# Kernel optimization log

Hardware: AMD Instinct MI355X
Metric: run time of the kernel (lower is better)

The kernel has to match this reference:

```python
import jax, jax.numpy as jnp
import numpy as np
import math

# ---------- real Clebsch-Gordan coupling tables (computed once, tiny) ----------
def _cg(j1, m1, j2, m2, j3, m3):
    if m1 + m2 != m3 or j3 < abs(j1 - j2) or j3 > j1 + j2:
        return 0.0
    f = math.factorial
    pre = ((2 * j3 + 1) * f(j3 + j1 - j2) * f(j3 - j1 + j2) * f(j1 + j2 - j3) / f(j1 + j2 + j3 + 1)) ** 0.5
    pre *= (f(j3 + m3) * f(j3 - m3) * f(j1 - m1) * f(j1 + m1) * f(j2 - m2) * f(j2 + m2)) ** 0.5
    s = 0.0
    for k in range(0, j1 + j2 - j3 + 1):
        d = (k, j1 + j2 - j3 - k, j1 - m1 - k, j2 + m2 - k, j3 - j2 + m1 + k, j3 - j1 - m2 + k)
        if min(d) < 0:
            continue
        den = 1
        for t in d:
            den *= f(t)
        s += (-1) ** k / den
    return pre * s

def _Q(l):  # complex->real spherical-harmonic change of basis
    Q = np.zeros((2 * l + 1, 2 * l + 1), dtype=complex)
    Q[l, l] = 1.0
    s = 2 ** -0.5
    for m in range(1, l + 1):
        Q[l + m, l + m] = (-1) ** m * s
        Q[l + m, l - m] = s
        Q[l - m, l + m] = -1j * (-1) ** m * s
        Q[l - m, l - m] = 1j * s
    return Q

def _K(l1, l2, l3):  # real coupling tensor [2l3+1, 2l1+1, 2l2+1]
    C = np.zeros((2 * l3 + 1, 2 * l1 + 1, 2 * l2 + 1), dtype=complex)
    for M3 in range(-l3, l3 + 1):
        for M1 in range(-l1, l1 + 1):
            for M2 in range(-l2, l2 + 1):
                C[M3 + l3, M1 + l1, M2 + l2] = _cg(l1, M1, l2, M2, l3, M3)
    K = np.einsum('cC,aA,bB,CAB->cab', _Q(l3).conj(), _Q(l1), _Q(l2), C)
    K = K.imag if np.abs(K.imag).max() > np.abs(K.real).max() else K.real
    return np.asarray(K, dtype=np.float32)

# the 9 'uvu' instructions (in_l, edge_l, out_l) with multiplicities (weight_numel=144)
_PATHS = [(0, 0, 0), (0, 2, 2), (1, 0, 1), (1, 2, 1), (1, 2, 2), (2, 0, 2), (2, 2, 0), (2, 2, 1), (2, 2, 2)]
_KT = [jnp.asarray(_K(*p)) for p in _PATHS]
_MULS = [32, 32, 16, 16, 16, 8, 8, 8, 8]
_SPLITS = np.cumsum(_MULS)[:-1].tolist()
NEI = 8
EPS = 1e-5

def _sh(u):  # component-normalized real SH of unit vectors, l=0..2 (m order -l..l, l=1 -> y,z,x)
    x, y, z = u[:, 0], u[:, 1], u[:, 2]
    sh0 = jnp.ones_like(x)[:, None]
    sh1 = np.float32(3 ** 0.5) * jnp.stack([y, z, x], -1)
    s15 = np.float32(15 ** 0.5)
    s5 = np.float32(5 ** 0.5)
    sh2 = jnp.stack([s15 * x * y, s15 * y * z, 0.5 * s5 * (3 * z * z - 1.0), s15 * x * z, 0.5 * s15 * (x * x - y * y)], -1)
    return sh0, sh1, sh2

def _path(xs, sh, wp, Kt):  # xs [E,u,2l1+1], sh [E,2l2+1], Kt [2l3+1,2l1+1,2l2+1] -> [E,u,2l3+1]
    return jnp.einsum('eui,ej,oij->euo', xs, sh, Kt) * wp[None, :, None]

def _layer(x0, x1, x2, pos, src, dst, w, W0, W1, W2, bw0, bb0, bw1, bw2, N):
    ev = pos[dst] - pos[src]
    u = ev / (jnp.linalg.norm(ev, axis=1, keepdims=True) + 1e-12)
    sh0, sh1, sh2 = _sh(u)
    s0 = x0[src][:, :, None]  # [E,32,1]
    s1 = x1[src]              # [E,16,3]
    s2 = x2[src]              # [E,8,5]
    ws = jnp.split(w, _SPLITS)
    p1 = _path(s0, sh0, ws[0], _KT[0])
    p2 = _path(s0, sh2, ws[1], _KT[1])
    p3 = _path(s1, sh0, ws[2], _KT[2])
    p4 = _path(s1, sh2, ws[3], _KT[3])
    p5 = _path(s1, sh2, ws[4], _KT[4])
    p6 = _path(s2, sh0, ws[5], _KT[5])
    p7 = _path(s2, sh2, ws[6], _KT[6])
    p8 = _path(s2, sh2, ws[7], _KT[7])
    p9 = _path(s2, sh2, ws[8], _KT[8])
    m0 = jnp.concatenate([p1, p7], 1)          # [E,40,1]
    m1 = jnp.concatenate([p3, p4, p8], 1)      # [E,40,3]
    m2 = jnp.concatenate([p2, p5, p6, p9], 1)  # [E,64,5]
    a0 = jax.ops.segment_sum(m0, dst, num_segments=N)
    a1 = jax.ops.segment_sum(m1, dst, num_segments=N)
    a2 = jax.ops.segment_sum(m2, dst, num_segments=N)
    y0 = (a0[:, :, 0] @ W0) * np.float32(1.0 / 40 ** 0.5)
    y1 = jnp.einsum('num,uv->nvm', a1, W1) * np.float32(1.0 / 40 ** 0.5)
    y2 = jnp.einsum('num,uv->nvm', a2, W2) * np.float32(1.0 / 64 ** 0.5)
    # equivariant batchnorm (training stats): scalars -> standard BN, l>0 -> norm BN
    f = y0 - y0.mean(0)
    y0 = f / jnp.sqrt((f * f).mean(0) + EPS) * bw0 + bb0
    y1 = y1 / jnp.sqrt((y1 * y1).mean(axis=(0, 2)) + EPS)[None, :, None] * bw1[None, :, None]
    y2 = y2 / jnp.sqrt((y2 * y2).mean(axis=(0, 2)) + EPS)[None, :, None] * bw2[None, :, None]
    return y0, y1, y2

def _forward(positions, W_emb, tp_w, lin_W0, lin_W1, lin_W2, bn_w0, bn_b0, bn_w1, bn_w2, Wf1, Wf2, bf2, Wf3, bf3):
    B, P, _ = positions.shape
    N = B * P
    pos = positions.reshape(N, 3)
    # kNN graph from dense cdist + topk (indices are not differentiated)
    pg = jax.lax.stop_gradient(pos)
    sq = jnp.sum(pg * pg, 1)
    d2 = sq[:, None] + sq[None, :] - 2.0 * (pg @ pg.T)
    _, idx = jax.lax.top_k(-d2, NEI + 1)  # smallest distances; col 0 is self
    src = jnp.repeat(jnp.arange(N), NEI)
    dst = idx[:, 1:].reshape(-1)
    x0 = jnp.ones((N, 1), jnp.float32) @ W_emb  # embedding: only 0e->0e path exists
    x1 = jnp.zeros((N, 16, 3), jnp.float32)
    x2 = jnp.zeros((N, 8, 5), jnp.float32)
    for l in range(3):
        y0, y1, y2 = _layer(x0, x1, x2, pos, src, dst, tp_w[l], lin_W0[l], lin_W1[l], lin_W2[l],
                            bn_w0[l], bn_b0[l], bn_w1[l], bn_w2[l], N)
        x0 = jax.nn.relu(y0) + x0
        x1 = jax.nn.relu(y1) + x1
        x2 = jax.nn.relu(y2) + x2
    h = jax.nn.relu((x0 @ Wf1) * np.float32(1.0 / 32 ** 0.5))  # scalar part -> 32x0e
    h = jax.nn.relu(h @ Wf2 + bf2)
    out = (h @ Wf3 + bf3).reshape(B, P, 2)
    return out

def setup_inputs() -> dict:
    key = jax.random.key(0)
    ks = jax.random.split(key, 16)
    B, P = 4, 2048
    return {
        'positions': jax.random.normal(ks[0], (B, P, 3), jnp.float32) * 3.0,
        'W_emb': jax.random.normal(ks[1], (1, 32), jnp.float32),
        'tp_w': jax.random.normal(ks[2], (3, 144), jnp.float32),
        'lin_W0': jax.random.normal(ks[3], (3, 40, 32), jnp.float32),
        'lin_W1': jax.random.normal(ks[4], (3, 40, 16), jnp.float32),
        'lin_W2': jax.random.normal(ks[5], (3, 64, 8), jnp.float32),
        'bn_w0': 1.0 + 0.05 * jax.random.normal(ks[6], (3, 32), jnp.float32),
        'bn_b0': jnp.zeros((3, 32), jnp.float32),
        'bn_w1': 1.0 + 0.05 * jax.random.normal(ks[7], (3, 16), jnp.float32),
        'bn_w2': 1.0 + 0.05 * jax.random.normal(ks[8], (3, 8), jnp.float32),
        'Wf1': jax.random.normal(ks[9], (32, 32), jnp.float32),
        'Wf2': jax.random.normal(ks[10], (32, 16), jnp.float32) * 0.2,
        'bf2': jax.random.normal(ks[11], (16,), jnp.float32) * 0.1,
        'Wf3': jax.random.normal(ks[12], (16, 2), jnp.float32) * 0.2,
        'bf3': jax.random.normal(ks[13], (2,), jnp.float32) * 0.1,
    }

def reference(positions, W_emb, tp_w, lin_W0, lin_W1, lin_W2, bn_w0, bn_b0, bn_w1, bn_w2, Wf1, Wf2, bf2, Wf3, bf3):
    return _forward(positions, W_emb, tp_w, lin_W0, lin_W1, lin_W2, bn_w0, bn_b0, bn_w1, bn_w2, Wf1, Wf2, bf2, Wf3, bf3)
```

## Files before the change

### kernel.cpp

```cpp
#include <hip/hip_runtime.h>
#include <math.h>

#define NN 8192
#define REV_CAP 48
#define KNN_CAP 384
#define PF 12

static const size_t OFF_K     = 0;
static const size_t OFF_CNT   = 512;
static const size_t OFF_REV   = 8704;
static const size_t OFF_STATS = 401920;
static const size_t OFF_XF    = 406528;
static const size_t OFF_YF    = 1389568;
static const size_t WS_FLOATS = 2372608;

__device__ double dfact(int n){ double r=1.0; for(int i=2;i<=n;++i) r*=(double)i; return r; }

__device__ double dcg(int j1,int m1,int j2,int m2,int j3,int m3){
  if (m1+m2!=m3) return 0.0;
  if (j3 < abs(j1-j2) || j3 > j1+j2) return 0.0;
  double pre = sqrt((double)(2*j3+1)*dfact(j3+j1-j2)*dfact(j3-j1+j2)*dfact(j1+j2-j3)/dfact(j1+j2+j3+1));
  pre *= sqrt(dfact(j3+m3)*dfact(j3-m3)*dfact(j1-m1)*dfact(j1+m1)*dfact(j2-m2)*dfact(j2+m2));
  double s=0.0;
  for(int k=0;k<=j1+j2-j3;++k){
    int d1=j1+j2-j3-k, d2=j1-m1-k, d3=j2+m2-k, d4=j3-j2+m1+k, d5=j3-j1-m2+k;
    if(d1<0||d2<0||d3<0||d4<0||d5<0) continue;
    double den = dfact(k)*dfact(d1)*dfact(d2)*dfact(d3)*dfact(d4)*dfact(d5);
    s += ((k&1)? -1.0: 1.0)/den;
  }
  return pre*s;
}

__device__ int qrow(int l,int r,int* col,double* re,double* im){
  const double s = 0.70710678118654752440;
  if (r==l){ col[0]=l; re[0]=1.0; im[0]=0.0; return 1; }
  if (r>l){ int m=r-l;
    col[0]=l+m; re[0]=((m&1)?-s:s); im[0]=0.0;
    col[1]=l-m; re[1]=s;            im[1]=0.0;
  } else { int m=l-r;
    col[0]=l+m; re[0]=0.0; im[0]=((m&1)? s : -s);
    col[1]=l-m; re[1]=0.0; im[1]=s;
  }
  return 2;
}

__global__ __launch_bounds__(256) void k_setup(const float* __restrict__ pos,
        const float* __restrict__ W_emb, float* __restrict__ Kbuf,
        float* __restrict__ xf,
        float* __restrict__ xs, float* __restrict__ ys, float* __restrict__ zs,
        float* __restrict__ qs,
        int* __restrict__ cnt, float* __restrict__ stats){
  int idx = blockIdx.x*256 + threadIdx.x;
  if (idx < 983040) { const int c = idx%120; xf[idx] = (c<32)? W_emb[c] : 0.f; return; }
  idx -= 983040;
  if (idx < 8192) {
    const float x=pos[3*idx], y=pos[3*idx+1], z=pos[3*idx+2];
    xs[idx]=x; ys[idx]=y; zs[idx]=z; qs[idx]=0.5f*(x*x+y*y+z*z);
    return;
  }
  idx -= 8192;
  if (idx < 8192) { cnt[idx]=0; return; }
  idx -= 8192;
  if (idx < 3072) { stats[idx]=0.f; return; }
  idx -= 3072;
  if (idx >= 405) return;

  const int tid = idx;
  const int sizes[9]={1,25,9,45,75,25,25,75,125};
  const int l1s[9]={0,0,1,1,1,2,2,2,2};
  const int l2s[9]={0,2,0,2,2,0,2,2,2};
  const int l3s[9]={0,2,1,1,2,2,0,1,2};
  int p=0, rem=tid;
  for(p=0;p<9;++p){ if(rem < sizes[p]) break; rem -= sizes[p]; }
  const int l1=l1s[p], l2=l2s[p], l3=l3s[p];
  const int n1=2*l1+1, n2=2*l2+1;
  const int c = rem/(n1*n2); const int r2 = rem%(n1*n2); const int a=r2/n2; const int b=r2%n2;

  int c3[2],c1[2],c2[2]; double re3[2],im3[2],re1[2],im1[2],re2[2],im2[2];
  const int nc3 = qrow(l3,c,c3,re3,im3);
  const int nc1 = qrow(l1,a,c1,re1,im1);
  const int nc2 = qrow(l2,b,c2,re2,im2);

  double accRe=0, accIm=0;
  for(int i3=0;i3<nc3;++i3){
    const double q3re=re3[i3], q3im=-im3[i3];
    for(int i1=0;i1<nc1;++i1){
      const double pre_re = q3re*re1[i1] - q3im*im1[i1];
      const double pre_im = q3re*im1[i1] + q3im*re1[i1];
      for(int i2=0;i2<nc2;++i2){
        const double cgv = dcg(l1, c1[i1]-l1, l2, c2[i2]-l2, l3, c3[i3]-l3);
        if (cgv==0.0) continue;
        accRe += (pre_re*re2[i2] - pre_im*im2[i2])*cgv;
        accIm += (pre_re*im2[i2] + pre_im*re2[i2])*cgv;
      }
    }
  }
  const bool useImag = ((l1+l2+l3)&1)!=0;
  Kbuf[tid] = (float)(useImag? accIm : accRe);
}

__device__ __forceinline__ unsigned fkey(float f){
  const unsigned b = __float_as_uint(f);
  return (b & 0x80000000u) ? ~b : (b | 0x80000000u);
}

#define RSELECT_PUSH(KMAX) do{ \
  unsigned P = 0u; int need = 9; \
  _Pragma("unroll 1") \
  for(int bit=31; bit>=0; --bit){ \
    const unsigned pref = P >> bit; \
    int c0 = 0; \
    _Pragma("unroll") \
    for(int k=0;k<KMAX;++k) c0 += __popcll(__ballot((ku[k]>>bit)==pref)); \
    if (need > c0){ need -= c0; P |= (1u<<bit); } \
  } \
  int c_eq = 0; \
  _Pragma("unroll") \
  for(int k=0;k<KMAX;++k) c_eq += __popcll(__ballot(ku[k]==P)); \
  bool tsel[KMAX]; \
  _Pragma("unroll") \
  for(int k=0;k<KMAX;++k) tsel[k] = (ku[k]==P); \
  if (c_eq > need){ \
    _Pragma("unroll") \
    for(int k=0;k<KMAX;++k) tsel[k]=false; \
    for(int r=0;r<need;++r){ \
      int mid = 0x7fffffff; \
      _Pragma("unroll") \
      for(int k=0;k<KMAX;++k) if (ku[k]==P && !tsel[k] && il[k]<mid) mid = il[k]; \
      _Pragma("unroll") \
      for(int s=32;s>0;s>>=1){ const int om = __shfl_xor(mid,s,64); mid = (om<mid)? om : mid; } \
      _Pragma("unroll") \
      for(int k=0;k<KMAX;++k) if (ku[k]==P && il[k]==mid) tsel[k]=true; \
    } \
  } \
  _Pragma("unroll") \
  for(int k=0;k<KMAX;++k){ \
    const bool take = (ku[k] < P) || tsel[k]; \
    const int ix = il[k]; \
    if (take && ix != node){ \
      int cpos = atomicAdd(&cnt[ix],1); \
      if (cpos < REV_CAP) rev[ix*REV_CAP + cpos] = node; \
    } \
  } \
}while(0)

__global__ __launch_bounds__(256, 8) void k_knn8(const float* __restrict__ xs,
                                              const float* __restrict__ ys,
                                              const float* __restrict__ zs,
                                              const float* __restrict__ qs,
                                              int* __restrict__ cnt, int* __restrict__ rev){
  const int lane = threadIdx.x & 63;
  const int w    = threadIdx.x >> 6;
  const int node = blockIdx.x*4 + w;
  __shared__ float sdist[4][KNN_CAP];
  __shared__ int   sidx[4][KNN_CAP];
  __shared__ int   scount[4];
  if (threadIdx.x < 4) scount[threadIdx.x]=0;
  __syncthreads();

  const float px = xs[node], py = ys[node], pz = zs[node];

  float m1 = INFINITY, m2 = INFINITY;
  for(int c=0;c<4;++c){
    const int base = (c*64 + lane)*4;
    const float4 fx = *(const float4*)(xs + base);
    const float4 fy = *(const float4*)(ys + base);
    const float4 fz = *(const float4*)(zs + base);
    const float4 fq = *(const float4*)(qs + base);
    float ss[4];
    ss[0] = fmaf(-px,fx.x, fmaf(-py,fy.x, fmaf(-pz,fz.x, fq.x)));
    ss[1] = fmaf(-px,fx.y, fmaf(-py,fy.y, fmaf(-pz,fz.y, fq.y)));
    ss[2] = fmaf(-px,fx.z, fmaf(-py,fy.z, fmaf(-pz,fz.z, fq.z)));
    ss[3] = fmaf(-px,fx.w, fmaf(-py,fy.w, fmaf(-pz,fz.w, fq.w)));
    #pragma unroll
    for(int q=0;q<4;++q){
      const float hi = fmaxf(m1, ss[q]);
      m1 = fminf(m1, ss[q]);
      m2 = fminf(m2, hi);
    }
  }
  {
    const unsigned kk1 = fkey(m1), kk2 = fkey(m2);
    unsigned P = 0u; int need = 9;
    #pragma unroll 1
    for(int bit=31; bit>=0; --bit){
      const unsigned pref = P >> bit;
      const int c0 = __popcll(__ballot((kk1>>bit)==pref)) + __popcll(__ballot((kk2>>bit)==pref));
      if (need > c0){ need -= c0; P |= (1u<<bit); }
    }
    m1 = __uint_as_float((P & 0x80000000u) ? (P & 0x7fffffffu) : ~P);
  }
  const float T = m1;

  {
    const int b0 = lane*4;
    float4 nfx = *(const float4*)(xs + b0);
    float4 nfy = *(const float4*)(ys + b0);
    float4 nfz = *(const float4*)(zs + b0);
    float4 nfq = *(const float4*)(qs + b0);
    for(int c=0;c<32;++c){
      const float4 fx=nfx, fy=nfy, fz=nfz, fq=nfq;
      const int cbase = (c*64 + lane)*4;
      if (c<31){
        const int nb2 = ((c+1)*64 + lane)*4;
        nfx = *(const float4*)(xs + nb2);
        nfy = *(const float4*)(ys + nb2);
        nfz = *(const float4*)(zs + nb2);
        nfq = *(const float4*)(qs + nb2);
      }
      float ss[4];
      ss[0] = fmaf(-px,fx.x, fmaf(-py,fy.x, fmaf(-pz,fz.x, fq.x)));
      ss[1] = fmaf(-px,fx.y, fmaf(-py,fy.y, fmaf(-pz,fz.y, fq.y)));
      ss[2] = fmaf(-px,fx.z, fmaf(-py,fy.z, fmaf(-pz,fz.z, fq.z)));
      ss[3] = fmaf(-px,fx.w, fmaf(-py,fy.w, fmaf(-pz,fz.w, fq.w)));
      #pragma unroll
      for(int q=0;q<4;++q){
        if (ss[q] <= T){
          int pos = atomicAdd(&scount[w],1);
          if (pos < KNN_CAP){ sdist[w][pos]=ss[q]; sidx[w][pos]=cbase+q; }
        }
      }
    }
  }
  __syncthreads();

  int m = scount[w]; if (m > KNN_CAP) m = KNN_CAP;
  unsigned ku[KNN_CAP/64]; int il[KNN_CAP/64];
  #pragma unroll
  for(int k=0;k<KNN_CAP/64;++k){
    const int j = lane + 64*k;
    if (j < m){ ku[k]=fkey(sdist[w][j]); il[k]=sidx[w][j]; }
    else      { ku[k]=0xffffffffu;       il[k]=0x7fffffff; }
  }
  if (m <= 128) RSELECT_PUSH(2);
  else          RSELECT_PUSH(6);
}

__global__ __launch_bounds__(256) void k_msg(
  const float* __restrict__ pos,
  const int* __restrict__ cnt, const int* __restrict__ rev,
  const float* __restrict__ Kbuf,
  const float* __restrict__ xf,
  const float* __restrict__ tpw,
  const float* __restrict__ W0, const float* __restrict__ W1, const float* __restrict__ W2,
  float* __restrict__ pA, float* __restrict__ pB,
  float* __restrict__ yf)
{
  const int t = threadIdx.x;
  const int w = t >> 6;
  const int lane = t & 63;
  const int n = blockIdx.x*4 + w;

  __shared__ float KL[405];
  __shared__ float TW[144];
  __shared__ float momP[4][120];
  __shared__ float momS[4][600];
  __shared__ float aS[4][480];
  __shared__ int   eIdx[4][REV_CAP];
  __shared__ float eSh[4][5][REV_CAP];
  __shared__ float bA[32], bB[96];
  for(int q=t;q<405;q+=256) KL[q]=Kbuf[q];
  for(int q=t;q<144;q+=256) TW[q]=tpw[q];
  if (t<96){ bB[t]=0.f; if(t<32) bA[t]=0.f; }

  const int deg0 = cnt[n];
  const int deg = (deg0<REV_CAP)? deg0 : REV_CAP;
  const float pnx=pos[3*n], pny=pos[3*n+1], pnz=pos[3*n+2];
  const float s15 = 3.8729833462f, s5c = 2.2360679775f;
  if (lane < deg){
    const int i = rev[n*REV_CAP+lane];
    eIdx[w][lane] = i;
    const float ex = pnx - pos[3*i], ey = pny - pos[3*i+1], ez = pnz - pos[3*i+2];
    const float rn = sqrtf(ex*ex+ey*ey+ez*ez) + 1e-12f;
    const float ux=ex/rn, uy=ey/rn, uz=ez/rn;
    eSh[w][0][lane]=s15*ux*uy;
    eSh[w][1][lane]=s15*uy*uz;
    eSh[w][2][lane]=0.5f*s5c*(3.f*uz*uz-1.f);
    eSh[w][3][lane]=s15*ux*uz;
    eSh[w][4][lane]=0.5f*s15*(ux*ux-uy*uy);
  }
  __syncthreads();

  const int c0 = lane*2;
  float mp0=0.f, mp1=0.f;
  float ms0[5], ms1[5];
  #pragma unroll
  for(int j=0;j<5;++j){ ms0[j]=0.f; ms1[j]=0.f; }

  int idxr[PF];
  #pragma unroll
  for(int k=0;k<PF;++k) idxr[k] = (k<deg)? eIdx[w][k] : 0;
  float2 fr[PF];
  if (lane<60){
    #pragma unroll
    for(int k=0;k<PF;++k) fr[k] = *(const float2*)(xf + (size_t)idxr[k]*120 + c0);
  }
  #pragma unroll
  for(int k=0;k<PF;++k){
    if (k<deg){
      const float sh0=eSh[w][0][k], sh1=eSh[w][1][k], sh2=eSh[w][2][k];
      const float sh3=eSh[w][3][k], sh4=eSh[w][4][k];
      if (lane<60){
        const float2 f = fr[k];
        mp0 += f.x; mp1 += f.y;
        ms0[0]+=f.x*sh0; ms0[1]+=f.x*sh1; ms0[2]+=f.x*sh2; ms0[3]+=f.x*sh3; ms0[4]+=f.x*sh4;
        ms1[0]+=f.y*sh0; ms1[1]+=f.y*sh1; ms1[2]+=f.y*sh2; ms1[3]+=f.y*sh3; ms1[4]+=f.y*sh4;
      }
    }
  }
  for(int e=PF;e<deg;++e){
    const int i = eIdx[w][e];
    const float sh0=eSh[w][0][e], sh1=eSh[w][1][e], sh2=eSh[w][2][e];
    const float sh3=eSh[w][3][e], sh4=eSh[w][4][e];
    if (lane<60){
      const float2 f = *(const float2*)(xf + (size_t)i*120 + c0);
      mp0 += f.x; mp1 += f.y;
      ms0[0]+=f.x*sh0; ms0[1]+=f.x*sh1; ms0[2]+=f.x*sh2; ms0[3]+=f.x*sh3; ms0[4]+=f.x*sh4;
      ms1[0]+=f.y*sh0; ms1[1]+=f.y*sh1; ms1[2]+=f.y*sh2; ms1[3]+=f.y*sh3; ms1[4]+=f.y*sh4;
    }
  }
  if (lane<60){
    momP[w][c0]=mp0; momP[w][c0+1]=mp1;
    #pragma unroll
    for(int j=0;j<5;++j){ momS[w][c0*5+j]=ms0[j]; momS[w][(c0+1)*5+j]=ms1[j]; }
  }
  __syncthreads();

  float acc[14];
  #pragma unroll
  for(int k=0;k<14;++k) acc[k]=0.f;

  if (lane<32){
    const int u=lane;
    const float rw0=TW[u], rw1=TW[32+u];
    acc[0] = rw0 * KL[0] * momP[w][u];
    float m0s[5];
    #pragma unroll
    for(int j=0;j<5;++j) m0s[j]=momS[w][u*5+j];
    #pragma unroll
    for(int o=0;o<5;++o){ float g=0.f;
      #pragma unroll
      for(int j=0;j<5;++j) g += KL[1+o*5+j]*m0s[j];
      acc[1+o] = rw1*g; }
  } else if (lane<48){
    const int u=lane-32;
    const float rw0=TW[64+u], rw1=TW[80+u], rw2=TW[96+u];
    float m1p[3], m1s[3][5];
    #pragma unroll
    for(int i=0;i<3;++i){
      m1p[i]=momP[w][32+u*3+i];
      #pragma unroll
      for(int j=0;j<5;++j) m1s[i][j]=momS[w][(32+u*3+i)*5+j];
    }
    #pragma unroll
    for(int o=0;o<3;++o){ float g=0.f;
      #pragma unroll
      for(int i=0;i<3;++i) g += KL[26+o*3+i]*m1p[i];
      acc[o]=rw0*g; }
    #pragma unroll
    for(int o=0;o<3;++o){ float g=0.f;
      #pragma unroll
      for(int i=0;i<3;++i)
        #pragma unroll
        for(int j=0;j<5;++j) g += KL[35+(o*3+i)*5+j]*m1s[i][j];
      acc[3+o]=rw1*g; }
    #pragma unroll
    for(int o=0;o<5;++o){ float g=0.f;
      #pragma unroll
      for(int i=0;i<3;++i)
        #pragma unroll
        for(int j=0;j<5;++j) g += KL[80+(o*3+i)*5+j]*m1s[i][j];
      acc[6+o]=rw2*g; }
  } else if (lane<56){
    const int u=lane-48;
    const float rw0=TW[112+u], rw1=TW[120+u], rw2=TW[128+u], rw3=TW[136+u];
    float m2p[5], m2s[5][5];
    #pragma unroll
    for(int i=0;i<5;++i){
      m2p[i]=momP[w][80+u*5+i];
      #pragma unroll
      for(int j=0;j<5;++j) m2s[i][j]=momS[w][(80+u*5+i)*5+j];
    }
    #pragma unroll
    for(int o=0;o<5;++o){ float g=0.f;
      #pragma unroll
      for(int i=0;i<5;++i) g += KL[155+o*5+i]*m2p[i];
      acc[o]=rw0*g; }
    { float g=0.f;
      #pragma unroll
      for(int i=0;i<5;++i)
        #pragma unroll
        for(int j=0;j<5;++j) g += KL[180+i*5+j]*m2s[i][j];
      acc[5]=rw1*g; }
    #pragma unroll
    for(int o=0;o<3;++o){ float g=0.f;
      #pragma unroll
      for(int i=0;i<5;++i)
        #pragma unroll
        for(int j=0;j<5;++j) g += KL[205+(o*5+i)*5+j]*m2s[i][j];
      acc[6+o]=rw2*g; }
    #pragma unroll
    for(int o=0;o<5;++o){ float g=0.f;
      #pragma unroll
      for(int i=0;i<5;++i)
        #pragma unroll
        for(int j=0;j<5;++j) g += KL[280+(o*5+i)*5+j]*m2s[i][j];
      acc[9+o]=rw3*g; }
  }

  if (lane<32){
    aS[w][lane] = acc[0];
    #pragma unroll
    for(int o=0;o<5;++o) aS[w][160 + lane*5+o] = acc[1+o];
  } else if (lane<48){
    const int uu=lane-32;
    #pragma unroll
    for(int m=0;m<3;++m){ aS[w][40 + uu*3+m] = acc[m]; aS[w][40 + (16+uu)*3+m] = acc[3+m]; }
    #pragma unroll
    for(int o=0;o<5;++o) aS[w][160 + (32+uu)*5+o] = acc[6+o];
  } else if (lane<56){
    const int uu=lane-48;
    aS[w][32+uu] = acc[5];
    #pragma unroll
    for(int m=0;m<3;++m) aS[w][40 + (32+uu)*3+m] = acc[6+m];
    #pragma unroll
    for(int o=0;o<5;++o){ aS[w][160 + (48+uu)*5+o] = acc[o]; aS[w][160 + (56+uu)*5+o] = acc[9+o]; }
  }
  __syncthreads();

  const float inv40 = 0.15811388300841896660f;
  for(int q=lane;q<120;q+=64){
    float out; int chan;
    if (q<32){
      float g=0.f;
      for(int uu=0;uu<40;++uu) g += aS[w][uu]*W0[uu*32+q];
      out = g*inv40; chan = q;
    } else if (q<80){
      const int e=q-32, v=e/3, m=e%3;
      float g=0.f;
      for(int uu=0;uu<40;++uu) g += aS[w][40+uu*3+m]*W1[uu*16+v];
      out = g*inv40; chan = 32+v;
    } else {
      const int e=q-80, tt=e/5, m=e%5;
      float g=0.f;
      for(int uu=0;uu<64;++uu) g += aS[w][160+uu*5+m]*W2[uu*8+tt];
      out = g*0.125f; chan = 48+tt;
    }
    yf[(size_t)n*120+q] = out;
    atomicAdd(&bB[chan], out*out);
    if (q<32) atomicAdd(&bA[q], out);
  }
  __syncthreads();
  if (t<96){
    const int slot = blockIdx.x & 7;
    atomicAdd(&pB[slot*96 + t], bB[t]);
    if (t<32) atomicAdd(&pA[slot*32 + t], bA[t]);
  }
}

__global__ __launch_bounds__(256) void k_norm(const float* __restrict__ yf,
                       const float* __restrict__ pA, const float* __restrict__ pB,
                       const float* __restrict__ bw0,const float* __restrict__ bb0,
                       const float* __restrict__ bw1,const float* __restrict__ bw2,
                       float* __restrict__ xf){
  __shared__ float sc[96], sf[32];
  const int t = threadIdx.x;
  if (t<96){
    float sB=0.f;
    #pragma unroll
    for(int k=0;k<8;++k) sB += pB[k*96+t];
    float scale;
    if (t<32){
      float sA=0.f;
      #pragma unroll
      for(int k=0;k<8;++k) sA += pA[k*32+t];
      const float mean = sA*(1.f/8192.f);
      const float var  = sB*(1.f/8192.f) - mean*mean;
      const float inv  = 1.f/sqrtf(var+1e-5f);
      scale = bw0[t]*inv;
      sf[t] = bb0[t] - mean*scale;
    } else if (t<48){
      scale = bw1[t-32]/sqrtf(sB*(1.f/(8192.f*3.f))+1e-5f);
    } else {
      scale = bw2[t-48]/sqrtf(sB*(1.f/(8192.f*5.f))+1e-5f);
    }
    sc[t]=scale;
  }
  __syncthreads();
  const int idx = blockIdx.x*256 + t;
  if (idx >= NN*120) return;
  const int c = idx%120;
  const int chan = (c<32)? c : ((c<80)? 32+(c-32)/3 : 48+(c-80)/5);
  const float v = yf[idx]*sc[chan] + ((c<32)? sf[c] : 0.f);
  xf[idx] += fmaxf(v,0.f);
}

__global__ __launch_bounds__(256) void k_normmlp(const float* __restrict__ yf,
                                             const float* __restrict__ xf,
                                             const float* __restrict__ pA, const float* __restrict__ pB,
                                             const float* __restrict__ bw0,const float* __restrict__ bb0,
                                             const float* __restrict__ Wf1,const float* __restrict__ Wf2,
                                             const float* __restrict__ bf2,const float* __restrict__ Wf3,
                                             const float* __restrict__ bf3, float* __restrict__ out){
  __shared__ float w1[1024], w2[512], w3[32], b2[16], b3[2], sc0[32], sf0[32];
  const int t=threadIdx.x;
  for(int q=t;q<1024;q+=256) w1[q]=Wf1[q];
  for(int q=t;q<512;q+=256)  w2[q]=Wf2[q];
  if(t<32) w3[t]=Wf3[t];
  if(t<16) b2[t]=bf2[t];
  if(t<2)  b3[t]=bf3[t];
  if(t<32){
    float sA=0.f, sB=0.f;
    #pragma unroll
    for(int k=0;k<8;++k){ sA += pA[k*32+t]; sB += pB[k*96+t]; }
    const float mean = sA*(1.f/8192.f);
    const float var  = sB*(1.f/8192.f) - mean*mean;
    const float inv  = 1.f/sqrtf(var+1e-5f);
    sc0[t] = bw0[t]*inv;
    sf0[t] = bb0[t] - mean*sc0[t];
  }
  __syncthreads();
  const int n = blockIdx.x*256+t;
  if(n>=NN) return;
  float xv[32];
  #pragma unroll
  for(int k=0;k<32;++k){
    const float v = yf[(size_t)n*120+k]*sc0[k] + sf0[k];
    xv[k] = xf[(size_t)n*120+k] + fmaxf(v,0.f);
  }
  const float inv32 = 0.17677669529663688110f;
  float h1[32];
  #pragma unroll 4
  for(int c=0;c<32;++c){ float g=0.f;
    #pragma unroll
    for(int k=0;k<32;++k) g+=xv[k]*w1[k*32+c];
    h1[c]=fmaxf(g*inv32,0.f); }
  float h2[16];
  #pragma unroll 4
  for(int c=0;c<16;++c){ float g=b2[c];
    #pragma unroll
    for(int k=0;k<32;++k) g+=h1[k]*w2[k*16+c];
    h2[c]=fmaxf(g,0.f); }
  #pragma unroll
  for(int m=0;m<2;++m){ float g=b3[m];
    #pragma unroll
    for(int k=0;k<16;++k) g+=h2[k]*w3[k*2+m];
    out[n*2+m]=g; }
}

extern "C" void kernel_launch(void* const* d_in, const int* in_sizes, int n_in,
                              void* d_out, int out_size, void* d_ws, size_t ws_size,
                              hipStream_t stream) {
  const float* positions = (const float*)d_in[0];
  const float* W_emb  = (const float*)d_in[1];
  const float* tp_w   = (const float*)d_in[2];
  const float* lin_W0 = (const float*)d_in[3];
  const float* lin_W1 = (const float*)d_in[4];
  const float* lin_W2 = (const float*)d_in[5];
  const float* bn_w0  = (const float*)d_in[6];
  const float* bn_b0  = (const float*)d_in[7];
  const float* bn_w1  = (const float*)d_in[8];
  const float* bn_w2  = (const float*)d_in[9];
  const float* Wf1 = (const float*)d_in[10];
  const float* Wf2 = (const float*)d_in[11];
  const float* bf2 = (const float*)d_in[12];
  const float* Wf3 = (const float*)d_in[13];
  const float* bf3 = (const float*)d_in[14];

  if (ws_size < WS_FLOATS*sizeof(float)) return;

  float* ws    = (float*)d_ws;
  float* Kbuf  = ws + OFF_K;
  int*   cnt   = (int*)(ws + OFF_CNT);
  int*   rev   = (int*)(ws + OFF_REV);
  float* stats = ws + OFF_STATS;
  float* xf = ws + OFF_XF;
  float* yf = ws + OFF_YF;

  float* xs = yf;
  float* ysA = yf + NN;
  float* zs = yf + 2*NN;
  float* qs = yf + 3*NN;

  k_setup<<<3918,256,0,stream>>>(positions, W_emb, Kbuf, xf, xs, ysA, zs, qs, cnt, stats);
  k_knn8<<<NN/4,256,0,stream>>>(xs, ysA, zs, qs, cnt, rev);

  for(int l=0;l<3;++l){
    float* pA = stats + l*1024;
    float* pB = pA + 256;
    k_msg<<<NN/4,256,0,stream>>>(positions, cnt, rev, Kbuf, xf,
                              tp_w + l*144, lin_W0 + l*40*32, lin_W1 + l*40*16, lin_W2 + l*64*8,
                              pA, pB, yf);
    if (l<2){
      k_norm<<<(NN*120+255)/256,256,0,stream>>>(yf, pA, pB,
                              bn_w0 + l*32, bn_b0 + l*32, bn_w1 + l*16, bn_w2 + l*8,
                              xf);
    }
  }
  k_normmlp<<<NN/256,256,0,stream>>>(yf, xf, stats + 2*1024, stats + 2*1024 + 256,
                              bn_w0 + 64, bn_b0 + 64,
                              Wf1, Wf2, bf2, Wf3, bf3, (float*)d_out);
}
```

Measured before the change: 287.2 us.

## Stage candidate point tiles in shared memory for all four waves in kNN

The kNN kernel now loads point coordinate tiles cooperatively into double-buffered shared memory, so the four waves in a block, each handling its own query node, share one global read instead of each streaming all 8192 points. The threshold-estimation pass over the first two tiles is folded into the same tile loop. This cuts global and L2 traffic by roughly four times. In exchange it adds a block-wide barrier per tile, uses more LDS, and drops the occupancy hint from the launch bounds.

```diff
diff --git a/kernel.cpp b/kernel.cpp
--- a/kernel.cpp
+++ b/kernel.cpp
@@ -5,6 +5,8 @@
 #define REV_CAP 48
 #define KNN_CAP 384
 #define PF 12
+#define TS 512
+#define NTILE 16
 
 static const size_t OFF_K     = 0;
 static const size_t OFF_CNT   = 512;
@@ -144,82 +146,92 @@
   } \
 }while(0)
 
-__global__ __launch_bounds__(256, 8) void k_knn8(const float* __restrict__ xs,
+__global__ __launch_bounds__(256) void k_knn8(const float* __restrict__ xs,
                                               const float* __restrict__ ys,
                                               const float* __restrict__ zs,
                                               const float* __restrict__ qs,
                                               int* __restrict__ cnt, int* __restrict__ rev){
-  const int lane = threadIdx.x & 63;
-  const int w    = threadIdx.x >> 6;
+  const int t256 = threadIdx.x;
+  const int lane = t256 & 63;
+  const int w    = t256 >> 6;
   const int node = blockIdx.x*4 + w;
+  __shared__ float tile[2][4*TS];
   __shared__ float sdist[4][KNN_CAP];
   __shared__ int   sidx[4][KNN_CAP];
   __shared__ int   scount[4];
-  if (threadIdx.x < 4) scount[threadIdx.x]=0;
-  __syncthreads();
+  if (t256 < 4) scount[t256]=0;
 
   const float px = xs[node], py = ys[node], pz = zs[node];
 
+  const int seg = t256 >> 7;
+  const int sub = t256 & 127;
+  const float* g0 = seg ? ys : xs;
+  const float* g1 = seg ? qs : zs;
+
   float m1 = INFINITY, m2 = INFINITY;
-  for(int c=0;c<4;++c){
-    const int base = (c*64 + lane)*4;
-    const float4 fx = *(const float4*)(xs + base);
-    const float4 fy = *(const float4*)(ys + base);
-    const float4 fz = *(const float4*)(zs + base);
-    const float4 fq = *(const float4*)(qs + base);
-    float ss[4];
-    ss[0] = fmaf(-px,fx.x, fmaf(-py,fy.x, fmaf(-pz,fz.x, fq.x)));
-    ss[1] = fmaf(-px,fx.y, fmaf(-py,fy.y, fmaf(-pz,fz.y, fq.y)));
-    ss[2] = fmaf(-px,fx.z, fmaf(-py,fy.z, fmaf(-pz,fz.z, fq.z)));
-    ss[3] = fmaf(-px,fx.w, fmaf(-py,fy.w, fmaf(-pz,fz.w, fq.w)));
-    #pragma unroll
-    for(int q=0;q<4;++q){
-      const float hi = fmaxf(m1, ss[q]);
-      m1 = fminf(m1, ss[q]);
-      m2 = fminf(m2, hi);
-    }
-  }
-  {
-    const unsigned kk1 = fkey(m1), kk2 = fkey(m2);
-    unsigned P = 0u; int need = 9;
-    #pragma unroll 1
-    for(int bit=31; bit>=0; --bit){
-      const unsigned pref = P >> bit;
-      const int c0 = __popcll(__ballot((kk1>>bit)==pref)) + __popcll(__ballot((kk2>>bit)==pref));
-      if (need > c0){ need -= c0; P |= (1u<<bit); }
-    }
-    m1 = __uint_as_float((P & 0x80000000u) ? (P & 0x7fffffffu) : ~P);
-  }
-  const float T = m1;
-
-  {
-    const int b0 = lane*4;
-    float4 nfx = *(const float4*)(xs + b0);
-    float4 nfy = *(const float4*)(ys + b0);
-    float4 nfz = *(const float4*)(zs + b0);
-    float4 nfq = *(const float4*)(qs + b0);
-    for(int c=0;c<32;++c){
-      const float4 fx=nfx, fy=nfy, fz=nfz, fq=nfq;
-      const int cbase = (c*64 + lane)*4;
-      if (c<31){
-        const int nb2 = ((c+1)*64 + lane)*4;
-        nfx = *(const float4*)(xs + nb2);
-        nfy = *(const float4*)(ys + nb2);
-        nfz = *(const float4*)(zs + nb2);
-        nfq = *(const float4*)(qs + nb2);
-      }
+  float T  = INFINITY;
+
+  float4 r0 = *(const float4*)(g0 + sub*4);
+  float4 r1 = *(const float4*)(g1 + sub*4);
+  *(float4*)(&tile[0][       seg*TS + sub*4]) = r0;
+  *(float4*)(&tile[0][2*TS + seg*TS + sub*4]) = r1;
+  int cur = 0;
+
+  for (int v = 0; v < NTILE+2; ++v){
+    const int vn = v+1;
+    if (vn < NTILE+2){
+      const int tn = (vn<2)? vn : vn-2;
+      r0 = *(const float4*)(g0 + tn*TS + sub*4);
+      r1 = *(const float4*)(g1 + tn*TS + sub*4);
+    }
+    __syncthreads();
+    const float* tb = tile[cur];
+    const int tt = (v<2)? v : v-2;
+    #pragma unroll
+    for (int qq=0; qq<TS/256; ++qq){
+      const int fo = (qq*64+lane)*4;
+      const float4 fx = *(const float4*)(tb + fo);
+      const float4 fy = *(const float4*)(tb +   TS + fo);
+      const float4 fz = *(const float4*)(tb + 2*TS + fo);
+      const float4 fq = *(const float4*)(tb + 3*TS + fo);
       float ss[4];
       ss[0] = fmaf(-px,fx.x, fmaf(-py,fy.x, fmaf(-pz,fz.x, fq.x)));
       ss[1] = fmaf(-px,fx.y, fmaf(-py,fy.y, fmaf(-pz,fz.y, fq.y)));
       ss[2] = fmaf(-px,fx.z, fmaf(-py,fy.z, fmaf(-pz,fz.z, fq.z)));
       ss[3] = fmaf(-px,fx.w, fmaf(-py,fy.w, fmaf(-pz,fz.w, fq.w)));
-      #pragma unroll
-      for(int q=0;q<4;++q){
-        if (ss[q] <= T){
-          int pos = atomicAdd(&scount[w],1);
-          if (pos < KNN_CAP){ sdist[w][pos]=ss[q]; sidx[w][pos]=cbase+q; }
+      if (v < 2){
+        #pragma unroll
+        for(int q=0;q<4;++q){
+          const float hi = fmaxf(m1, ss[q]);
+          m1 = fminf(m1, ss[q]);
+          m2 = fminf(m2, hi);
+        }
+      } else {
+        #pragma unroll
+        for(int q=0;q<4;++q){
+          if (ss[q] <= T){
+            int pos = atomicAdd(&scount[w],1);
+            if (pos < KNN_CAP){ sdist[w][pos]=ss[q]; sidx[w][pos]=tt*TS + fo + q; }
+          }
         }
       }
+    }
+    if (v == 1){
+      const unsigned kk1 = fkey(m1), kk2 = fkey(m2);
+      unsigned P = 0u; int need = 9;
+      #pragma unroll 1
+      for(int bit=31; bit>=0; --bit){
+        const unsigned pref = P >> bit;
+        const int c0 = __popcll(__ballot((kk1>>bit)==pref)) + __popcll(__ballot((kk2>>bit)==pref));
+        if (need > c0){ need -= c0; P |= (1u<<bit); }
+      }
+      T = __uint_as_float((P & 0x80000000u) ? (P & 0x7fffffffu) : ~P);
+    }
+    if (vn < NTILE+2){
+      float* db = tile[cur^1];
+      *(float4*)(db +        seg*TS + sub*4) = r0;
+      *(float4*)(db + 2*TS + seg*TS + sub*4) = r1;
+      cur ^= 1;
     }
   }
   __syncthreads();
```

After: 292.3 us. Within noise of the previous version (+1.8%).
